# Kernel tuning notes

Hardware: AMD Instinct MI355X
Metric: run time of the kernel (lower is better)

The kernel has to match this reference:

```python
import jax, jax.numpy as jnp
import numpy as np

B, S, E, H = 2, 2048, 1024, 16
D = E // H  # head_dim = 64


def setup_inputs() -> dict:
    key = jax.random.key(0)
    ks = jax.random.split(key, 4)
    return {
        "hidden_states": jax.random.normal(ks[0], (B, S, E), jnp.float32),
        "qk_weight": jax.random.normal(ks[1], (E, 2 * E), jnp.float32) * 0.02,
        "qk_bias": jnp.zeros((2 * E,), jnp.float32),
        "v_weight": jax.random.normal(ks[2], (E, E), jnp.float32) * 0.02,
        "v_resid_gain": jnp.ones((), jnp.float32),
        "v_skip_gain": jnp.ones((), jnp.float32),
        "proj_weight": jax.random.normal(ks[3], (E, E), jnp.float32) * 0.02,
        "proj_resid_gain": jnp.ones((), jnp.float32),
        "proj_skip_gain": jnp.ones((), jnp.float32),
        "attn_mat_resid_gain": jnp.ones((H,), jnp.float32),
        "attn_mat_skip_gain": jnp.ones((H,), jnp.float32),
        "centre_attn_gain": jnp.ones((H,), jnp.float32),
    }


def reference(hidden_states, qk_weight, qk_bias, v_weight, v_resid_gain,
              v_skip_gain, proj_weight, proj_resid_gain, proj_skip_gain,
              attn_mat_resid_gain, attn_mat_skip_gain, centre_attn_gain):
    b, s, e = hidden_states.shape
    dt = hidden_states.dtype
    eye_e = jnp.eye(e, dtype=dt)

    # qk_attn: MyConv1D (standard linear), split into query/key
    qk = hidden_states @ qk_weight + qk_bias
    q, k = jnp.split(qk, 2, axis=-1)
    # v_attn: skip MyConv1D -> x @ (resid_gain * W + skip_gain * I), no bias
    v = hidden_states @ (v_resid_gain * v_weight + v_skip_gain * eye_e)

    def split_heads(t):  # [b,s,e] -> [b,h,s,d]
        return t.reshape(b, s, H, D).transpose(0, 2, 1, 3)

    q, k, v = split_heads(q), split_heads(k), split_heads(v)

    # scaled causal attention scores
    scores = jnp.einsum('bhqd,bhkd->bhqk', q, k) / jnp.asarray(D, dt) ** 0.5
    causal = jnp.tril(jnp.ones((s, s), bool))
    scores = jnp.where(causal, scores, jnp.finfo(dt).min)
    attn = jax.nn.softmax(scores, axis=-1)

    # shaped attention: gain-mix softmax probs with identity and causal-uniform
    uniform = jnp.tril(jnp.ones((s, s), dt) / jnp.arange(1, s + 1, dtype=dt)[:, None])
    g_r = attn_mat_resid_gain[None, :, None, None]
    g_s = attn_mat_skip_gain[None, :, None, None]
    g_c = centre_attn_gain[None, :, None, None]
    new_attn = g_r * attn + g_s * jnp.eye(s, dtype=dt) - g_c * uniform

    ctx = jnp.einsum('bhqk,bhkd->bhqd', new_attn, v)
    ctx = ctx.transpose(0, 2, 1, 3).reshape(b, s, e)  # merge heads
    # c_proj: skip MyConv1D, no bias
    out = ctx @ (proj_resid_gain * proj_weight + proj_skip_gain * eye_e)
    return out
```

## Files before the change

### kernel.cpp

```cpp
#include <hip/hip_runtime.h>

typedef __bf16 bf16;
typedef __attribute__((ext_vector_type(8))) __bf16 bf16x8;
typedef __attribute__((ext_vector_type(4))) float f32x4;

union U16x8 { uint4 u; bf16 h[8]; };
union Pack4 { uint2 u2; bf16 h[4]; };

#define QSCALE 0.18033688011112042f

__device__ __forceinline__ void async16(const bf16* g, bf16* l) {
    __builtin_amdgcn_global_load_lds((const __attribute__((address_space(1))) void*)g,
                                     (__attribute__((address_space(3))) void*)l, 16, 0, 0);
}

__device__ const int QT_OF[40] = {15,15,15,15,14,14,14,14,13,13,13,13,12,12,12,12,
                                  11,11,11,10,10,10,9,9,9,8,8,8,7,7,6,6,5,5,4,4,3,2,1,0};
__device__ const int CK_OF[40] = {0,1,2,3,0,1,2,3,0,1,2,3,0,1,2,3,
                                  0,1,2,0,1,2,0,1,2,0,1,2,0,1,0,1,0,1,0,1,0,0,0,0};
__device__ const int BASE_OF[16] = {39,38,37,36,34,32,30,28,25,22,19,16,12,8,4,0};

__global__ void prep(const float* __restrict__ hs, bf16* __restrict__ hsb,
                     const float* __restrict__ qkw, const float* __restrict__ vw,
                     const float* __restrict__ pw, bf16* __restrict__ qkvT,
                     bf16* __restrict__ pwT,
                     const float* __restrict__ vrg, const float* __restrict__ vsg,
                     const float* __restrict__ prg, const float* __restrict__ psg) {
    const int K = 1024;
    int bx = blockIdx.x;
    if (bx < 4096) {
        int i = (bx * 256 + threadIdx.x) * 4;
        float4 f = *(const float4*)(hs + i);
        hsb[i + 0] = (bf16)f.x; hsb[i + 1] = (bf16)f.y;
        hsb[i + 2] = (bf16)f.z; hsb[i + 3] = (bf16)f.w;
        return;
    }
    int r = bx - 4096;
    int z = r < 2048 ? 0 : (r < 3072 ? 1 : 2);
    int q = z == 0 ? r : (z == 1 ? r - 2048 : r - 3072);
    int ntiles = z == 0 ? 64 : 32;
    int N = z == 0 ? 2048 : 1024;
    const float* W = z == 0 ? qkw : (z == 1 ? vw : pw);
    bf16* WT = z == 0 ? qkvT : (z == 1 ? qkvT + (size_t)2 * 1024 * 1024 : pwT);
    float g0 = z == 0 ? 1.f : (z == 1 ? vrg[0] : prg[0]);
    float g1 = z == 0 ? 0.f : (z == 1 ? vsg[0] : psg[0]);

    __shared__ float tile[32][33];
    int n0 = (q % ntiles) * 32, k0 = (q / ntiles) * 32;
    int tx = threadIdx.x & 31, ty = threadIdx.x >> 5;
    #pragma unroll
    for (int rr = 0; rr < 32; rr += 8)
        tile[ty + rr][tx] = W[(size_t)(k0 + ty + rr) * N + n0 + tx];
    __syncthreads();
    #pragma unroll
    for (int rr = 0; rr < 32; rr += 8) {
        int n = n0 + ty + rr, k = k0 + tx;
        float v = g0 * tile[tx][ty + rr] + ((n == k) ? g1 : 0.f);
        if (z == 0 && n < 1024) v *= QSCALE;
        WT[(size_t)n * K + k] = (bf16)v;
    }
}

template<int BN>
__global__ __launch_bounds__(256, 3)
void gemm_bt(const bf16* __restrict__ A, const bf16* __restrict__ BT,
             int M, int N, int K, void* __restrict__ Cout, bf16* __restrict__ C2,
             bf16* __restrict__ C2T, float* __restrict__ csum,
             int mode, const float* __restrict__ aux) {
    __shared__ __align__(16) bf16 As[128][64];
    __shared__ __align__(16) bf16 Bs[BN][64];
    constexpr int JF = BN / 32;
    int m0 = blockIdx.y * 128, n0 = blockIdx.x * BN;
    int t = threadIdx.x, lane = t & 63, w = t >> 6;
    int wm = (w >> 1) * 64, wn = (w & 1) * (BN / 2);
    int lrow = lane & 15, lkg = lane >> 4;

    f32x4 acc[4][JF] = {};

    int gsw = ((lane & 7) ^ ((lane >> 3) & 7)) * 8;
    const bf16* Ab = A + (size_t)(m0 + w * 8 + (lane >> 3)) * K + gsw;
    const bf16* Bb = BT + (size_t)(n0 + w * 8 + (lane >> 3)) * K + gsw;

    for (int k0 = 0; k0 < K; k0 += 64) {
        #pragma unroll
        for (int p = 0; p < 4; p++)
            async16(Ab + (size_t)(p * 32) * K + k0, &As[p * 32 + w * 8][0]);
        #pragma unroll
        for (int p = 0; p < BN / 32; p++)
            async16(Bb + (size_t)(p * 32) * K + k0, &Bs[p * 32 + w * 8][0]);
        __syncthreads();
        #pragma unroll
        for (int ks = 0; ks < 2; ks++) {
            bf16x8 af[4], bfr[JF];
            int phys = (((4 * ks + lkg) ^ (lrow & 7)) << 3);
            #pragma unroll
            for (int i = 0; i < 4; i++) af[i] = *(const bf16x8*)&As[wm + i * 16 + lrow][phys];
            #pragma unroll
            for (int j = 0; j < JF; j++) bfr[j] = *(const bf16x8*)&Bs[wn + j * 16 + lrow][phys];
            #pragma unroll
            for (int i = 0; i < 4; i++)
                #pragma unroll
                for (int j = 0; j < JF; j++)
                    acc[i][j] = __builtin_amdgcn_mfma_f32_16x16x32_bf16(af[i], bfr[j], acc[i][j], 0, 0, 0);
        }
        __syncthreads();
    }

    int rgrp = (lane >> 4) * 4;
    #pragma unroll
    for (int i = 0; i < 4; i++) {
        #pragma unroll
        for (int j = 0; j < JF; j++) {
            int col = n0 + wn + j * 16 + lrow;
            int row0 = m0 + wm + i * 16 + rgrp;
            if (mode == 0) {
                if (col < 2048) {
                    float bb = aux[col];
                    if (col < 1024) bb *= QSCALE;
                    #pragma unroll
                    for (int reg = 0; reg < 4; reg++)
                        ((bf16*)Cout)[(size_t)(row0 + reg) * 2048 + col] = (bf16)(acc[i][j][reg] + bb);
                } else {
                    int c = col - 2048;
                    Pack4 p4;
                    #pragma unroll
                    for (int reg = 0; reg < 4; reg++) {
                        bf16 hv = (bf16)acc[i][j][reg];
                        C2[(size_t)(row0 + reg) * 1024 + c] = hv;
                        p4.h[reg] = hv;
                    }
                    *(uint2*)&C2T[(size_t)c * 4096 + row0] = p4.u2;
                }
            } else {
                #pragma unroll
                for (int reg = 0; reg < 4; reg++)
                    ((float*)Cout)[(size_t)(row0 + reg) * N + col] = acc[i][j][reg];
            }
        }
    }

    if (mode == 0 && n0 >= 2048) {
        int chunk = (m0 + wm) >> 6;
        #pragma unroll
        for (int j = 0; j < JF; j++) {
            float s = 0.f;
            #pragma unroll
            for (int i = 0; i < 4; i++)
                #pragma unroll
                for (int reg = 0; reg < 4; reg++) s += acc[i][j][reg];
            s += __shfl_xor(s, 16, 64);
            s += __shfl_xor(s, 32, 64);
            if (lkg == 0)
                atomicAdd(&csum[(size_t)chunk * 1024 + (n0 - 2048 + wn + j * 16 + lrow)], s);
        }
    }
}

__global__ __launch_bounds__(256, 3)
void flash_split(const bf16* __restrict__ qk, const bf16* __restrict__ vT,
                 bf16* __restrict__ Opart, float* __restrict__ lbuf,
                 int S, int E, int H) {
    __shared__ __align__(16) bf16 Ks[2][64][64];
    __shared__ __align__(16) bf16 Vt[2][64][64];
    __shared__ __align__(16) bf16 Ps[4][32][72];

    int item = blockIdx.x, bh = blockIdx.y;
    int qt = QT_OF[item], ck = CK_OF[item];
    int b = bh >> 4, h = bh & 15;
    int q0 = qt * 128;
    int ktstart = ck * 8;
    int nloc = min(8, 2 * (qt + 1) - ktstart);
    int t = threadIdx.x, lane = t & 63, w = t >> 6;
    int lrow = lane & 15, lkg = lane >> 4;
    const int ld = 2 * E;

    const bf16* Qg  = qk + (size_t)(b * S + q0) * ld + h * 64;
    const bf16* Kg0 = qk + (size_t)(b * S) * ld + E + h * 64;
    const bf16* Vg0 = vT + (size_t)(h * 64) * 4096 + b * 2048;

    bf16x8 qf[2][2];
    #pragma unroll
    for (int qg = 0; qg < 2; qg++)
        #pragma unroll
        for (int ks = 0; ks < 2; ks++)
            qf[qg][ks] = *(const bf16x8*)&Qg[(size_t)(32 * w + 16 * qg + lrow) * ld + ks * 32 + lkg * 8];

    f32x4 oacc[4][2] = {};
    float lrun[2] = {0.f, 0.f};

    auto stage = [&](int buf, int kt) {
        int k0 = kt * 64;
        int g = (lane & 7) ^ ((lane >> 3) & 7);
        #pragma unroll
        for (int p = 0; p < 2; p++) {
            int row = w * 8 + p * 32 + (lane >> 3);
            async16(Kg0 + (size_t)(k0 + row) * ld + g * 8, &Ks[buf][row][(lane & 7) * 8]);
            async16(Vg0 + (size_t)row * 4096 + k0 + g * 8, &Vt[buf][row][(lane & 7) * 8]);
        }
    };

    stage(0, ktstart);
    for (int kl = 0; kl < nloc; kl++) {
        int buf = kl & 1;
        int k0 = (ktstart + kl) * 64;
        __syncthreads();
        if (kl + 1 < nloc) stage(1 - buf, ktstart + kl + 1);

        bool skip0 = (k0 > q0 + 32 * w + 15);
        bool skip1 = (k0 > q0 + 32 * w + 31);
        if (skip0 && skip1) continue;

        f32x4 sacc[2][4] = {};
        #pragma unroll
        for (int ks = 0; ks < 2; ks++) {
            bf16x8 ak[4];
            int phys = (((4 * ks + lkg) ^ (lrow & 7)) << 3);
            #pragma unroll
            for (int kf = 0; kf < 4; kf++)
                ak[kf] = *(const bf16x8*)&Ks[buf][16 * kf + lrow][phys];
            #pragma unroll
            for (int kf = 0; kf < 4; kf++)
                sacc[0][kf] = __builtin_amdgcn_mfma_f32_16x16x32_bf16(ak[kf], qf[0][ks], sacc[0][kf], 0, 0, 0);
            if (!skip1)
                #pragma unroll
                for (int kf = 0; kf < 4; kf++)
                    sacc[1][kf] = __builtin_amdgcn_mfma_f32_16x16x32_bf16(ak[kf], qf[1][ks], sacc[1][kf], 0, 0, 0);
        }

        #pragma unroll
        for (int qg = 0; qg < 2; qg++) {
            if ((qg == 0 && skip0) || (qg == 1 && skip1)) continue;
            int kmin = q0 + 32 * w + 16 * qg;
            bool diag = (k0 + 63 > kmin);
            int qrow = kmin + lrow;
            float rsum = 0.f;
            #pragma unroll
            for (int kf = 0; kf < 4; kf++) {
                Pack4 p4;
                #pragma unroll
                for (int r = 0; r < 4; r++) {
                    float sv = sacc[qg][kf][r];
                    if (diag && (k0 + 16 * kf + 4 * lkg + r > qrow)) sv = -1e30f;
                    float p = exp2f(sv);
                    rsum += p;
                    p4.h[r] = (bf16)p;
                }
                *(uint2*)&Ps[w][16 * qg + lrow][16 * kf + 4 * lkg] = p4.u2;
            }
            lrun[qg] += rsum;
        }

        #pragma unroll
        for (int ks = 0; ks < 2; ks++) {
            bf16x8 av[4];
            int phys = (((4 * ks + lkg) ^ (lrow & 7)) << 3);
            #pragma unroll
            for (int df = 0; df < 4; df++)
                av[df] = *(const bf16x8*)&Vt[buf][16 * df + lrow][phys];
            #pragma unroll
            for (int qg = 0; qg < 2; qg++) {
                if ((qg == 0 && skip0) || (qg == 1 && skip1)) continue;
                bf16x8 bp = *(const bf16x8*)&Ps[w][16 * qg + lrow][ks * 32 + lkg * 8];
                #pragma unroll
                for (int df = 0; df < 4; df++)
                    oacc[df][qg] = __builtin_amdgcn_mfma_f32_16x16x32_bf16(av[df], bp, oacc[df][qg], 0, 0, 0);
            }
        }
    }

    size_t ibase = (size_t)(bh * 40 + item) * 128;
    #pragma unroll
    for (int qg = 0; qg < 2; qg++) {
        #pragma unroll
        for (int df = 0; df < 4; df++) {
            Pack4 p4;
            #pragma unroll
            for (int r = 0; r < 4; r++) p4.h[r] = (bf16)oacc[df][qg][r];
            *(uint2*)&Ps[w][16 * qg + lrow][16 * df + 4 * lkg] = p4.u2;
        }
        float l = lrun[qg];
        l += __shfl_xor(l, 16, 64);
        l += __shfl_xor(l, 32, 64);
        if (lkg == 0) lbuf[ibase + w * 32 + qg * 16 + lrow] = l;
    }
    int r_l = lane >> 1, half = lane & 1;
    bf16* orow = Opart + (ibase + w * 32 + r_l) * 64 + 32 * half;
    #pragma unroll
    for (int c = 0; c < 4; c++)
        *(uint4*)&orow[8 * c] = *(const uint4*)&Ps[w][r_l][32 * half + 8 * c];
}

__global__ void merge_combine(const bf16* __restrict__ Opart, const float* __restrict__ lbuf,
                              const bf16* __restrict__ v, const float* __restrict__ csum,
                              const float* __restrict__ gr, const float* __restrict__ gs,
                              const float* __restrict__ gc, bf16* __restrict__ ctx) {
    const int S = 2048, E = 1024;
    int qt = blockIdx.x, bh = blockIdx.y;
    int b = bh >> 4, h = bh & 15;
    int nc = (qt >> 2) + 1, base = BASE_OF[qt];
    int q0 = qt * 128;
    int t = threadIdx.x;

    __shared__ bf16 osm[128][66];

    {
        int r = t >> 1, dh = (t & 1) * 32;
        float L = 0.f;
        for (int c = 0; c < nc; c++)
            L += lbuf[(size_t)(bh * 40 + base + c) * 128 + r];
        float inv = 1.f / L;
        float o[32] = {};
        for (int c = 0; c < nc; c++) {
            const bf16* src = Opart + ((size_t)(bh * 40 + base + c) * 128 + r) * 64 + dh;
            #pragma unroll
            for (int g = 0; g < 4; g++) {
                U16x8 u; u.u = *(const uint4*)&src[g * 8];
                #pragma unroll
                for (int j = 0; j < 8; j++) o[g * 8 + j] += (float)u.h[j];
            }
        }
        #pragma unroll
        for (int j = 0; j < 32; j++) osm[r][dh + j] = (bf16)(o[j] * inv);
    }
    __syncthreads();

    if (t < 128) {
        int c = t & 63, ckk = t >> 6;
        int col = h * 64 + c;
        float grh = gr[h], gsh = gs[h], gch = gc[h];
        int chunk = (q0 >> 6) + ckk;
        float run = 0.f;
        for (int j = 0; j < chunk; j++)
            run += csum[((size_t)b * 32 + j) * E + col];
        const bf16* vp = v + ((size_t)b * S + chunk * 64) * E + col;
        bf16* cp = ctx + ((size_t)b * S + chunk * 64) * E + col;
        for (int i = 0; i < 64; i++) {
            int row = chunk * 64 + i;
            float vv = (float)vp[(size_t)i * E];
            run += vv;
            float pm = run / (float)(row + 1);
            cp[(size_t)i * E] = (bf16)(grh * (float)osm[ckk * 64 + i][c] + gsh * vv - gch * pm);
        }
    }
}

extern "C" void kernel_launch(void* const* d_in, const int* in_sizes, int n_in,
                              void* d_out, int out_size, void* d_ws, size_t ws_size,
                              hipStream_t stream) {
    const float* hs  = (const float*)d_in[0];
    const float* qkw = (const float*)d_in[1];
    const float* qkb = (const float*)d_in[2];
    const float* vw  = (const float*)d_in[3];
    const float* vrg = (const float*)d_in[4];
    const float* vsg = (const float*)d_in[5];
    const float* pw  = (const float*)d_in[6];
    const float* prg = (const float*)d_in[7];
    const float* psg = (const float*)d_in[8];
    const float* amr = (const float*)d_in[9];
    const float* ams = (const float*)d_in[10];
    const float* amc = (const float*)d_in[11];
    float* out = (float*)d_out;

    const int B = 2, S = 2048, E = 1024, H = 16, M = B * S;
    char* ws = (char*)d_ws;
    size_t off = 0;
    auto alloc = [&](size_t bytes) { void* p = ws + off; off += (bytes + 255) & ~255ull; return p; };
    bf16* hsb   = (bf16*)alloc((size_t)M * E * 2);
    bf16* qkvT  = (bf16*)alloc((size_t)3 * E * E * 2);
    bf16* pwT   = (bf16*)alloc((size_t)E * E * 2);
    bf16* qko   = (bf16*)alloc((size_t)M * 2 * E * 2);
    bf16* vo    = (bf16*)alloc((size_t)M * E * 2);
    bf16* vT    = (bf16*)alloc((size_t)E * M * 2);
    float* csum = (float*)alloc((size_t)B * 32 * E * 4);
    bf16* ctxb  = (bf16*)alloc((size_t)M * E * 2);
    bf16* Opart = (bf16*)alloc((size_t)32 * 40 * 128 * 64 * 2);
    float* lbuf = (float*)alloc((size_t)32 * 40 * 128 * 4);

    hipMemsetAsync(csum, 0, (size_t)B * 32 * E * 4, stream);
    prep<<<8192, 256, 0, stream>>>(hs, hsb, qkw, vw, pw, qkvT, pwT, vrg, vsg, prg, psg);

    gemm_bt<128><<<dim3(3 * E / 128, M / 128), 256, 0, stream>>>(
        hsb, qkvT, M, 3 * E, E, qko, vo, vT, csum, 0, qkb);

    flash_split<<<dim3(40, 32), 256, 0, stream>>>(qko, vT, Opart, lbuf, S, E, H);
    merge_combine<<<dim3(16, 32), 256, 0, stream>>>(Opart, lbuf, vo, csum, amr, ams, amc, ctxb);

    gemm_bt<64><<<dim3(E / 64, M / 128), 256, 0, stream>>>(
        ctxb, pwT, M, E, E, out, nullptr, nullptr, nullptr, 2, nullptr);
}
```

Before: 216.5 us.

## Drop row-major V output, fold csum zeroing into prep, remap GEMM blocks

The QKV GEMM no longer writes the row-major V copy. merge_combine now reads V from the transposed buffer with vector loads and uses all 256 threads over 32-row sub-chunks, with column sums kept at 32-row granularity. The csum memset moves into extra blocks of the prep kernel, removing a separate launch. GEMM launches switch to a 1D grid whose block mapping interleaves M tiles across consecutive blocks to change cache locality. In exchange there are twice as many csum atomics and partial sums to accumulate in the prefix loop.

```diff
diff --git a/kernel.cpp b/kernel.cpp
--- a/kernel.cpp
+++ b/kernel.cpp
@@ -23,19 +23,25 @@
 __global__ void prep(const float* __restrict__ hs, bf16* __restrict__ hsb,
                      const float* __restrict__ qkw, const float* __restrict__ vw,
                      const float* __restrict__ pw, bf16* __restrict__ qkvT,
-                     bf16* __restrict__ pwT,
+                     bf16* __restrict__ pwT, float* __restrict__ csum,
                      const float* __restrict__ vrg, const float* __restrict__ vsg,
                      const float* __restrict__ prg, const float* __restrict__ psg) {
     const int K = 1024;
     int bx = blockIdx.x;
-    if (bx < 4096) {
-        int i = (bx * 256 + threadIdx.x) * 4;
+    if (bx < 8) {
+        float4* p = (float4*)csum + (bx * 256 + threadIdx.x) * 16;
+        #pragma unroll
+        for (int i = 0; i < 16; i++) p[i] = make_float4(0.f, 0.f, 0.f, 0.f);
+        return;
+    }
+    if (bx < 4104) {
+        int i = ((bx - 8) * 256 + threadIdx.x) * 4;
         float4 f = *(const float4*)(hs + i);
         hsb[i + 0] = (bf16)f.x; hsb[i + 1] = (bf16)f.y;
         hsb[i + 2] = (bf16)f.z; hsb[i + 3] = (bf16)f.w;
         return;
     }
-    int r = bx - 4096;
+    int r = bx - 4104;
     int z = r < 2048 ? 0 : (r < 3072 ? 1 : 2);
     int q = z == 0 ? r : (z == 1 ? r - 2048 : r - 3072);
     int ntiles = z == 0 ? 64 : 32;
@@ -64,13 +70,16 @@
 template<int BN>
 __global__ __launch_bounds__(256, 3)
 void gemm_bt(const bf16* __restrict__ A, const bf16* __restrict__ BT,
-             int M, int N, int K, void* __restrict__ Cout, bf16* __restrict__ C2,
+             int M, int N, int K, void* __restrict__ Cout,
              bf16* __restrict__ C2T, float* __restrict__ csum,
              int mode, const float* __restrict__ aux) {
     __shared__ __align__(16) bf16 As[128][64];
     __shared__ __align__(16) bf16 Bs[BN][64];
     constexpr int JF = BN / 32;
-    int m0 = blockIdx.y * 128, n0 = blockIdx.x * BN;
+    int bid = blockIdx.x;
+    int g32 = bid & 31;
+    int m0 = ((g32 & 7) * 4 + (g32 >> 3)) * 128;
+    int n0 = (bid >> 5) * BN;
     int t = threadIdx.x, lane = t & 63, w = t >> 6;
     int wm = (w >> 1) * 64, wn = (w & 1) * (BN / 2);
     int lrow = lane & 15, lkg = lane >> 4;
@@ -124,11 +133,7 @@
                     int c = col - 2048;
                     Pack4 p4;
                     #pragma unroll
-                    for (int reg = 0; reg < 4; reg++) {
-                        bf16 hv = (bf16)acc[i][j][reg];
-                        C2[(size_t)(row0 + reg) * 1024 + c] = hv;
-                        p4.h[reg] = hv;
-                    }
+                    for (int reg = 0; reg < 4; reg++) p4.h[reg] = (bf16)acc[i][j][reg];
                     *(uint2*)&C2T[(size_t)c * 4096 + row0] = p4.u2;
                 }
             } else {
@@ -140,18 +145,22 @@
     }
 
     if (mode == 0 && n0 >= 2048) {
-        int chunk = (m0 + wm) >> 6;
+        int chunkb = (m0 + wm) >> 5;
         #pragma unroll
         for (int j = 0; j < JF; j++) {
-            float s = 0.f;
-            #pragma unroll
-            for (int i = 0; i < 4; i++)
-                #pragma unroll
-                for (int reg = 0; reg < 4; reg++) s += acc[i][j][reg];
-            s += __shfl_xor(s, 16, 64);
-            s += __shfl_xor(s, 32, 64);
-            if (lkg == 0)
-                atomicAdd(&csum[(size_t)chunk * 1024 + (n0 - 2048 + wn + j * 16 + lrow)], s);
+            float s0 = 0.f, s1 = 0.f;
+            #pragma unroll
+            for (int reg = 0; reg < 4; reg++) {
+                s0 += acc[0][j][reg] + acc[1][j][reg];
+                s1 += acc[2][j][reg] + acc[3][j][reg];
+            }
+            s0 += __shfl_xor(s0, 16, 64); s0 += __shfl_xor(s0, 32, 64);
+            s1 += __shfl_xor(s1, 16, 64); s1 += __shfl_xor(s1, 32, 64);
+            if (lkg == 0) {
+                int col = n0 - 2048 + wn + j * 16 + lrow;
+                atomicAdd(&csum[(size_t)chunkb * 1024 + col], s0);
+                atomicAdd(&csum[(size_t)(chunkb + 1) * 1024 + col], s1);
+            }
         }
     }
 }
@@ -291,7 +300,7 @@
 }
 
 __global__ void merge_combine(const bf16* __restrict__ Opart, const float* __restrict__ lbuf,
-                              const bf16* __restrict__ v, const float* __restrict__ csum,
+                              const bf16* __restrict__ vT, const float* __restrict__ csum,
                               const float* __restrict__ gr, const float* __restrict__ gs,
                               const float* __restrict__ gc, bf16* __restrict__ ctx) {
     const int S = 2048, E = 1024;
@@ -324,22 +333,26 @@
     }
     __syncthreads();
 
-    if (t < 128) {
-        int c = t & 63, ckk = t >> 6;
+    {
+        int c = t & 63, sc = t >> 6;
         int col = h * 64 + c;
+        int row0 = q0 + sc * 32;
         float grh = gr[h], gsh = gs[h], gch = gc[h];
-        int chunk = (q0 >> 6) + ckk;
         float run = 0.f;
-        for (int j = 0; j < chunk; j++)
-            run += csum[((size_t)b * 32 + j) * E + col];
-        const bf16* vp = v + ((size_t)b * S + chunk * 64) * E + col;
-        bf16* cp = ctx + ((size_t)b * S + chunk * 64) * E + col;
-        for (int i = 0; i < 64; i++) {
-            int row = chunk * 64 + i;
-            float vv = (float)vp[(size_t)i * E];
-            run += vv;
-            float pm = run / (float)(row + 1);
-            cp[(size_t)i * E] = (bf16)(grh * (float)osm[ckk * 64 + i][c] + gsh * vv - gch * pm);
+        int cend = qt * 4 + sc;
+        for (int j = 0; j < cend; j++)
+            run += csum[((size_t)b * 64 + j) * E + col];
+        const bf16* vrow = vT + (size_t)col * 4096 + b * 2048 + row0;
+        U16x8 vv[4];
+        #pragma unroll
+        for (int g = 0; g < 4; g++) vv[g].u = *(const uint4*)&vrow[g * 8];
+        bf16* cp = ctx + ((size_t)(b * S + row0)) * E + col;
+        #pragma unroll
+        for (int i = 0; i < 32; i++) {
+            float v = (float)vv[i >> 3].h[i & 7];
+            run += v;
+            float pm = run / (float)(row0 + i + 1);
+            cp[(size_t)i * E] = (bf16)(grh * (float)osm[sc * 32 + i][c] + gsh * v - gch * pm);
         }
     }
 }
@@ -369,22 +382,20 @@
     bf16* qkvT  = (bf16*)alloc((size_t)3 * E * E * 2);
     bf16* pwT   = (bf16*)alloc((size_t)E * E * 2);
     bf16* qko   = (bf16*)alloc((size_t)M * 2 * E * 2);
-    bf16* vo    = (bf16*)alloc((size_t)M * E * 2);
     bf16* vT    = (bf16*)alloc((size_t)E * M * 2);
-    float* csum = (float*)alloc((size_t)B * 32 * E * 4);
+    float* csum = (float*)alloc((size_t)128 * E * 4);
     bf16* ctxb  = (bf16*)alloc((size_t)M * E * 2);
     bf16* Opart = (bf16*)alloc((size_t)32 * 40 * 128 * 64 * 2);
     float* lbuf = (float*)alloc((size_t)32 * 40 * 128 * 4);
 
-    hipMemsetAsync(csum, 0, (size_t)B * 32 * E * 4, stream);
-    prep<<<8192, 256, 0, stream>>>(hs, hsb, qkw, vw, pw, qkvT, pwT, vrg, vsg, prg, psg);
-
-    gemm_bt<128><<<dim3(3 * E / 128, M / 128), 256, 0, stream>>>(
-        hsb, qkvT, M, 3 * E, E, qko, vo, vT, csum, 0, qkb);
+    prep<<<8200, 256, 0, stream>>>(hs, hsb, qkw, vw, pw, qkvT, pwT, csum, vrg, vsg, prg, psg);
+
+    gemm_bt<128><<<32 * (3 * E / 128), 256, 0, stream>>>(
+        hsb, qkvT, M, 3 * E, E, qko, vT, csum, 0, qkb);
 
     flash_split<<<dim3(40, 32), 256, 0, stream>>>(qko, vT, Opart, lbuf, S, E, H);
-    merge_combine<<<dim3(16, 32), 256, 0, stream>>>(Opart, lbuf, vo, csum, amr, ams, amc, ctxb);
-
-    gemm_bt<64><<<dim3(E / 64, M / 128), 256, 0, stream>>>(
-        ctxb, pwT, M, E, E, out, nullptr, nullptr, nullptr, 2, nullptr);
-}
+    merge_combine<<<dim3(16, 32), 256, 0, stream>>>(Opart, lbuf, vT, csum, amr, ams, amc, ctxb);
+
+    gemm_bt<64><<<32 * (E / 64), 256, 0, stream>>>(
+        ctxb, pwT, M, E, E, out, nullptr, nullptr, 2, nullptr);
+}
```

Result: faster. 209.4 us (-3.3%).
